# Kernel tuning notes

Measured on AMD Instinct MI355X. Metric: run time of the kernel, lower is better.

Reference implementation:

```python
import jax, jax.numpy as jnp
import numpy as np

B, S, EMB, HID, IMG, ATT, K, HL = 64, 512, 768, 512, 2048, 512, 6, 20


def setup_inputs() -> dict:
    key = jax.random.key(0)
    ks = jax.random.split(key, 14)
    u = lambda k, shape: jax.random.uniform(k, shape, jnp.float32, -0.1, 0.1)
    return {
        "representations": jax.random.normal(ks[0], (B, S, EMB), jnp.float32),
        "lengths": jax.random.randint(ks[1], (B,), 0, S),
        "separate_images": jax.random.normal(ks[2], (B, K, IMG), jnp.float32),
        "visual_context": jax.random.normal(ks[3], (B, K * IMG), jnp.float32),
        "prev_hist": jax.random.normal(ks[4], (B, K, HL, EMB), jnp.float32),
        "hist_counts": jax.random.randint(ks[5], (B, K), 0, HL + 1),
        "masks": jax.random.randint(ks[6], (B, S, 1), 0, 2).astype(bool),
        "W_sep": u(ks[7], (IMG, HID)), "b_sep": jnp.zeros((HID,), jnp.float32),
        "W_e2h": u(ks[8], (EMB, HID)), "b_e2h": jnp.zeros((HID,), jnp.float32),
        "W_hist": u(ks[9], (EMB, HID)), "b_hist": jnp.zeros((HID,), jnp.float32),
        "W_ctx": u(ks[10], (K * IMG, HID)), "b_ctx": jnp.zeros((HID,), jnp.float32),
        "W_mm": u(ks[11], (2 * HID, HID)), "b_mm": jnp.zeros((HID,), jnp.float32),
        "W_a1": u(ks[12], (HID, ATT)), "b_a1": jnp.zeros((ATT,), jnp.float32),
        "W_a2": u(ks[13], (ATT, 1)), "b_a2": jnp.zeros((1,), jnp.float32),
    }


def reference(representations, lengths, separate_images, visual_context,
              prev_hist, hist_counts, masks,
              W_sep, b_sep, W_e2h, b_e2h, W_hist, b_hist, W_ctx, b_ctx,
              W_mm, b_mm, W_a1, b_a1, W_a2, b_a2):
    # dropout_prob = 0 -> dropout is identity (eval-mode equivalence)
    input_reps = jax.nn.relu(representations @ W_e2h + b_e2h)          # [B,S,H]
    ctx = jax.nn.relu(visual_context @ W_ctx + b_ctx)                  # [B,H]
    ctx_rep = jnp.broadcast_to(ctx[:, None, :], input_reps.shape)
    mm = jax.nn.relu(jnp.concatenate([input_reps, ctx_rep], -1) @ W_mm + b_mm)  # [B,S,H]
    scores = jnp.tanh(mm @ W_a1 + b_a1) @ W_a2 + b_a2                  # [B,S,1]
    scores = jnp.where(masks, -jnp.inf, scores)
    att_w = jax.nn.softmax(scores, axis=1)                             # softmax over seq
    attended = jnp.sum(mm * att_w, axis=1)                             # [B,H]

    sep = separate_images @ W_sep + b_sep                              # [B,K,H]
    hl = prev_hist.shape[2]
    valid = jnp.arange(hl)[None, None, :] < hist_counts[:, :, None]    # [B,K,HL]
    hsum = jnp.sum(prev_hist * valid[..., None].astype(prev_hist.dtype), axis=2)
    havg = hsum / jnp.maximum(hist_counts, 1)[..., None].astype(prev_hist.dtype)
    hproj = jax.nn.relu(havg @ W_hist + b_hist)                        # [B,K,H]
    sep = sep + jnp.where((hist_counts > 0)[..., None], hproj, 0.0)
    sep = jax.nn.relu(sep)
    # F.normalize(p=2, dim=2, eps=1e-12)
    sep = sep / jnp.maximum(jnp.linalg.norm(sep, axis=2, keepdims=True), 1e-12)
    dot = jnp.einsum('bkh,bh->bk', sep, attended)[..., None]           # [B,K,1]
    return dot
```

## Files before the change

kernel.cpp:

```cpp
#include <hip/hip_runtime.h>
#include <math.h>

#define B_    64
#define S_    512
#define EMB_  768
#define HID_  512
#define IMG_  2048
#define ATT_  512
#define K_    6
#define HL_   20

typedef __attribute__((ext_vector_type(8))) short bf16x8;
typedef __attribute__((ext_vector_type(4))) float f32x4;

__device__ __forceinline__ unsigned short f2b(float f) {
    unsigned int u = __float_as_uint(f);
    u += 0x7fffu + ((u >> 16) & 1u);
    return (unsigned short)(u >> 16);
}
__device__ __forceinline__ float b2f(unsigned short s) {
    return __uint_as_float(((unsigned int)s) << 16);
}

#define GLD_LDS16(gp, lp)                                                        \
    __builtin_amdgcn_global_load_lds(                                            \
        (const __attribute__((address_space(1))) void*)(gp),                     \
        (__attribute__((address_space(3))) void*)(lp), 16, 0, 0)

__global__ __launch_bounds__(256)
void mask_detect(const unsigned char* __restrict__ m, int* __restrict__ flag, int nbytes) {
    __shared__ int found;
    if (threadIdx.x == 0) found = 0;
    __syncthreads();
    for (int i = threadIdx.x; i < nbytes; i += 256) {
        if ((i & 3) != 0 && m[i] != 0) found = 1;
    }
    __syncthreads();
    if (threadIdx.x == 0) *flag = found;
}

__global__ __launch_bounds__(256)
void cvt_f32_bf16(const float* __restrict__ in, unsigned short* __restrict__ out, int n8) {
    int stride = gridDim.x * 256;
    for (int i = blockIdx.x * 256 + threadIdx.x; i < n8; i += stride) {
        float4 a = ((const float4*)in)[i * 2];
        float4 b = ((const float4*)in)[i * 2 + 1];
        unsigned short r[8] = {f2b(a.x), f2b(a.y), f2b(a.z), f2b(a.w),
                               f2b(b.x), f2b(b.y), f2b(b.z), f2b(b.w)};
        ((uint4*)out)[i] = *(uint4*)r;
    }
}

__global__ __launch_bounds__(256)
void transpose_cvt(const float* __restrict__ W, unsigned short* __restrict__ Wt,
                   int Kd, int N) {
    __shared__ float tile[32][33];
    int k0 = blockIdx.x * 32, n0 = blockIdx.y * 32;
    int tx = threadIdx.x & 31, ty = threadIdx.x >> 5;
    #pragma unroll
    for (int i = 0; i < 4; ++i)
        tile[ty + i * 8][tx] = W[(size_t)(k0 + ty + i * 8) * N + n0 + tx];
    __syncthreads();
    #pragma unroll
    for (int i = 0; i < 4; ++i)
        Wt[(size_t)(n0 + ty + i * 8) * Kd + k0 + tx] = f2b(tile[tx][ty + i * 8]);
}

template<int ACT>
__global__ __launch_bounds__(256)
void gemm_bf16(const unsigned short* __restrict__ A, const unsigned short* __restrict__ Bt,
               const float* __restrict__ bias, const float* __restrict__ row_add,
               int row_div, unsigned short* __restrict__ Co, int M, int N, int Kd) {
    __shared__ unsigned short Als[2][128 * 64];
    __shared__ unsigned short Bls[2][128 * 64];
    const int tid = threadIdx.x;

    const int nwg = gridDim.x;
    const int cpx = nwg >> 3;
    const int lid = ((int)blockIdx.x & 7) * cpx + ((int)blockIdx.x >> 3);
    const int ntl = N >> 7;
    const int bn = (lid % ntl) << 7;
    const int bm = (lid / ntl) << 7;

    const int lane = tid & 63;
    const int wid = tid >> 6;
    const int wr = wid >> 1, wc = wid & 1;
    const int fr = lane & 15, hi = lane >> 4;

    f32x4 acc[4][4] = {};

    int srow[4], scol[4];
    #pragma unroll
    for (int c = 0; c < 4; ++c) {
        int g = c * 256 + tid;
        srow[c] = g >> 3;
        scol[c] = (g & 7) ^ (srow[c] & 7);
    }

    const int nt = Kd >> 6;
    #pragma unroll
    for (int c = 0; c < 4; ++c) {
        int g = c * 256 + tid;
        GLD_LDS16(A + (size_t)(bm + srow[c]) * Kd + scol[c] * 8, &Als[0][g * 8]);
        GLD_LDS16(Bt + (size_t)(bn + srow[c]) * Kd + scol[c] * 8, &Bls[0][g * 8]);
    }
    __syncthreads();

    for (int t = 0; t < nt; ++t) {
        const int buf = t & 1;
        if (t + 1 < nt) {
            const int k0 = (t + 1) << 6;
            #pragma unroll
            for (int c = 0; c < 4; ++c) {
                int g = c * 256 + tid;
                GLD_LDS16(A + (size_t)(bm + srow[c]) * Kd + k0 + scol[c] * 8,
                          &Als[buf ^ 1][g * 8]);
                GLD_LDS16(Bt + (size_t)(bn + srow[c]) * Kd + k0 + scol[c] * 8,
                          &Bls[buf ^ 1][g * 8]);
            }
        }
        #pragma unroll
        for (int kk = 0; kk < 2; ++kk) {
            bf16x8 af[4], bv[4];
            #pragma unroll
            for (int m = 0; m < 4; ++m) {
                int row = wr * 64 + m * 16 + fr;
                int sc = (kk * 4 + hi) ^ (fr & 7);
                af[m] = *(const bf16x8*)&Als[buf][row * 64 + sc * 8];
            }
            #pragma unroll
            for (int n = 0; n < 4; ++n) {
                int row = wc * 64 + n * 16 + fr;
                int sc = (kk * 4 + hi) ^ (fr & 7);
                bv[n] = *(const bf16x8*)&Bls[buf][row * 64 + sc * 8];
            }
            #pragma unroll
            for (int m = 0; m < 4; ++m)
                #pragma unroll
                for (int n = 0; n < 4; ++n)
                    acc[m][n] = __builtin_amdgcn_mfma_f32_16x16x32_bf16(af[m], bv[n], acc[m][n], 0, 0, 0);
        }
        __syncthreads();
    }

    const int rg = hi;
    #pragma unroll
    for (int m = 0; m < 4; ++m) {
        #pragma unroll
        for (int n = 0; n < 4; ++n) {
            int col = bn + wc * 64 + n * 16 + fr;
            float badd = bias ? bias[col] : 0.f;
            #pragma unroll
            for (int r = 0; r < 4; ++r) {
                int row = bm + wr * 64 + m * 16 + rg * 4 + r;
                float x = acc[m][n][r] + badd;
                if (row_add) x += row_add[(size_t)(row / row_div) * N + col];
                if (ACT == 1) x = fmaxf(x, 0.f);
                if (ACT == 2) x = tanhf(x);
                Co[(size_t)row * N + col] = f2b(x);
            }
        }
    }
}

__global__ __launch_bounds__(256)
void gemm_splitk(const float* __restrict__ A, const float* __restrict__ W,
                 float* __restrict__ P, int M, int N, int Kd, int kps) {
    __shared__ float As[16][68];
    __shared__ float Ws[16][64];
    const int tid = threadIdx.x;
    const int bm = blockIdx.y * 64, bn = blockIdx.x * 64;
    const int ks = blockIdx.z;
    const int tx = tid & 15, ty = tid >> 4;
    const int arow = tid >> 2, akq = tid & 3;
    const int wk = tid >> 4, wnq = tid & 15;

    float acc[4][4] = {};
    const int kbeg = ks * kps, kend = kbeg + kps;

    for (int k0 = kbeg; k0 < kend; k0 += 16) {
        float4 av = *(const float4*)&A[(size_t)(bm + arow) * Kd + k0 + akq * 4];
        float4 wv = *(const float4*)&W[(size_t)(k0 + wk) * N + bn + wnq * 4];
        As[akq * 4 + 0][arow] = av.x;
        As[akq * 4 + 1][arow] = av.y;
        As[akq * 4 + 2][arow] = av.z;
        As[akq * 4 + 3][arow] = av.w;
        *(float4*)&Ws[wk][wnq * 4] = wv;
        __syncthreads();
        #pragma unroll
        for (int kk = 0; kk < 16; ++kk) {
            float4 a4 = *(const float4*)&As[kk][ty * 4];
            float4 b4 = *(const float4*)&Ws[kk][tx * 4];
            float a_[4] = {a4.x, a4.y, a4.z, a4.w};
            float b_[4] = {b4.x, b4.y, b4.z, b4.w};
            #pragma unroll
            for (int i = 0; i < 4; ++i)
                #pragma unroll
                for (int j = 0; j < 4; ++j)
                    acc[i][j] += a_[i] * b_[j];
        }
        __syncthreads();
    }

    float* Pbase = P + (size_t)ks * M * N;
    #pragma unroll
    for (int i = 0; i < 4; ++i) {
        int row = bm + ty * 4 + i;
        float4 v = {acc[i][0], acc[i][1], acc[i][2], acc[i][3]};
        *(float4*)&Pbase[(size_t)row * N + bn + tx * 4] = v;
    }
}

template<int ACT>
__global__ __launch_bounds__(256)
void reduce_k(const float* __restrict__ P, const float* __restrict__ bias,
              float* __restrict__ C, int MN, int N, int nsplit) {
    int idx = blockIdx.x * 256 + threadIdx.x;
    if (idx >= MN) return;
    float s = 0.f;
    for (int z = 0; z < nsplit; ++z) s += P[(size_t)z * MN + idx];
    if (bias) s += bias[idx & (N - 1)];
    if (ACT == 1) s = fmaxf(s, 0.f);
    C[idx] = s;
}

__global__ __launch_bounds__(256)
void score_dot(const unsigned short* __restrict__ t, const float* __restrict__ W_a2,
               const float* __restrict__ b_a2, float* __restrict__ scores) {
    int row = blockIdx.x * 4 + (threadIdx.x >> 6);
    int lane = threadIdx.x & 63;
    const unsigned short* tr = t + (size_t)row * ATT_;
    float s = 0.f;
    #pragma unroll
    for (int i = 0; i < ATT_ / 64; ++i)
        s += b2f(tr[lane + i * 64]) * W_a2[lane + i * 64];
    #pragma unroll
    for (int off = 32; off; off >>= 1) s += __shfl_down(s, off, 64);
    if (lane == 0) scores[row] = s + b_a2[0];
}

__global__ __launch_bounds__(256)
void softmax_mask(float* __restrict__ scores, const void* __restrict__ masks_raw,
                  const int* __restrict__ flag) {
    int b = blockIdx.x, tid = threadIdx.x;
    bool isb = (*flag) != 0;
    const unsigned char* mb = (const unsigned char*)masks_raw;
    const int* mi = (const int*)masks_raw;
    int lane = tid & 63, wv = tid >> 6;
    __shared__ float red[4], red2[4];

    float m = -INFINITY;
    for (int s = tid; s < S_; s += 256) {
        int idx = b * S_ + s;
        bool mk = isb ? (mb[idx] != 0) : (mi[idx] != 0);
        float v = mk ? -INFINITY : scores[idx];
        scores[idx] = v;
        m = fmaxf(m, v);
    }
    #pragma unroll
    for (int off = 32; off; off >>= 1) m = fmaxf(m, __shfl_down(m, off, 64));
    if (lane == 0) red[wv] = m;
    __syncthreads();
    if (tid == 0) red[0] = fmaxf(fmaxf(red[0], red[1]), fmaxf(red[2], red[3]));
    __syncthreads();
    float Mx = red[0];

    float sum = 0.f;
    for (int s = tid; s < S_; s += 256) {
        int idx = b * S_ + s;
        float e = expf(scores[idx] - Mx);
        scores[idx] = e;
        sum += e;
    }
    #pragma unroll
    for (int off = 32; off; off >>= 1) sum += __shfl_down(sum, off, 64);
    if (lane == 0) red2[wv] = sum;
    __syncthreads();
    if (tid == 0) red2[0] = red2[0] + red2[1] + red2[2] + red2[3];
    __syncthreads();
    float inv = 1.f / red2[0];
    for (int s = tid; s < S_; s += 256) scores[b * S_ + s] *= inv;
}

__global__ __launch_bounds__(256)
void attended_k(const unsigned short* __restrict__ mm, const float* __restrict__ att_w,
                float* __restrict__ attended) {
    int b = blockIdx.x;
    int h = blockIdx.y * 256 + threadIdx.x;
    __shared__ float w[S_];
    for (int s = threadIdx.x; s < S_; s += 256) w[s] = att_w[b * S_ + s];
    __syncthreads();
    float acc = 0.f;
    for (int s = 0; s < S_; ++s)
        acc += b2f(mm[((size_t)b * S_ + s) * HID_ + h]) * w[s];
    attended[b * HID_ + h] = acc;
}

__global__ __launch_bounds__(256)
void hist_avg(const float* __restrict__ ph, const int* __restrict__ hcnt,
              float* __restrict__ havg) {
    int bk = blockIdx.x;
    int cnt = hcnt[bk];
    float denom = (float)(cnt > 1 ? cnt : 1);
    const float* base = ph + (size_t)bk * HL_ * EMB_;
    for (int e = threadIdx.x; e < EMB_; e += 256) {
        float s = 0.f;
        for (int l = 0; l < cnt; ++l) s += base[l * EMB_ + e];
        havg[bk * EMB_ + e] = s / denom;
    }
}

__global__ __launch_bounds__(256)
void combine(const float* __restrict__ sep0, const float* __restrict__ hproj,
             const int* __restrict__ hcnt, const float* __restrict__ attended,
             float* __restrict__ out) {
    int bk = blockIdx.x, tid = threadIdx.x;
    int b = bk / K_;
    int cnt = hcnt[bk];
    float sq = 0.f, dt = 0.f;
    #pragma unroll
    for (int i = 0; i < HID_ / 256; ++i) {
        int h = tid + i * 256;
        float v = sep0[bk * HID_ + h];
        if (cnt > 0) v += hproj[bk * HID_ + h];
        v = fmaxf(v, 0.f);
        sq += v * v;
        dt += v * attended[b * HID_ + h];
    }
    #pragma unroll
    for (int off = 32; off; off >>= 1) {
        sq += __shfl_down(sq, off, 64);
        dt += __shfl_down(dt, off, 64);
    }
    __shared__ float rs[4], rd[4];
    int lane = tid & 63, wv = tid >> 6;
    if (lane == 0) { rs[wv] = sq; rd[wv] = dt; }
    __syncthreads();
    if (tid == 0) {
        float Sq = rs[0] + rs[1] + rs[2] + rs[3];
        float Dt = rd[0] + rd[1] + rd[2] + rd[3];
        float norm = fmaxf(sqrtf(Sq), 1e-12f);
        out[bk] = Dt / norm;
    }
}

extern "C" void kernel_launch(void* const* d_in, const int* in_sizes, int n_in,
                              void* d_out, int out_size, void* d_ws, size_t ws_size,
                              hipStream_t stream) {
    const float* reps     = (const float*)d_in[0];
    const float* sep_imgs = (const float*)d_in[2];
    const float* vctx     = (const float*)d_in[3];
    const float* phist    = (const float*)d_in[4];
    const int*   hcnt     = (const int*)d_in[5];
    const void*  masks    = d_in[6];
    const float* W_sep = (const float*)d_in[7];
    const float* b_sep = (const float*)d_in[8];
    const float* W_e2h = (const float*)d_in[9];
    const float* b_e2h = (const float*)d_in[10];
    const float* W_hist = (const float*)d_in[11];
    const float* b_hist = (const float*)d_in[12];
    const float* W_ctx = (const float*)d_in[13];
    const float* b_ctx = (const float*)d_in[14];
    const float* W_mm = (const float*)d_in[15];
    const float* b_mm = (const float*)d_in[16];
    const float* W_a1 = (const float*)d_in[17];
    const float* b_a1 = (const float*)d_in[18];
    const float* W_a2 = (const float*)d_in[19];
    const float* b_a2 = (const float*)d_in[20];
    float* out = (float*)d_out;

    const size_t MS = (size_t)B_ * S_;

    unsigned short* repsb = (unsigned short*)d_ws;
    unsigned short* actA  = repsb + MS * EMB_;
    unsigned short* actB  = actA + MS * HID_;
    unsigned short* WtE2H = actB + MS * HID_;
    unsigned short* WtMM  = WtE2H + (size_t)EMB_ * HID_;
    unsigned short* WtA1  = WtMM + (size_t)HID_ * HID_;
    float* skbuf = (float*)(WtA1 + (size_t)HID_ * HID_);
    float* ctx   = skbuf + (size_t)16 * 384 * 512;
    float* ctx2  = ctx + B_ * HID_;
    float* scores = ctx2 + B_ * HID_;
    float* attended = scores + MS;
    float* sep0  = attended + B_ * HID_;
    float* havg  = sep0 + B_ * K_ * HID_;
    float* hproj = havg + B_ * K_ * EMB_;
    int*   flag  = (int*)(hproj + B_ * K_ * HID_);

    mask_detect<<<1, 256, 0, stream>>>((const unsigned char*)masks, flag, 8192);

    cvt_f32_bf16<<<2048, 256, 0, stream>>>(reps, repsb, (int)(MS * EMB_ / 8));
    transpose_cvt<<<dim3(EMB_ / 32, HID_ / 32), 256, 0, stream>>>(W_e2h, WtE2H, EMB_, HID_);
    transpose_cvt<<<dim3(HID_ / 32, HID_ / 32), 256, 0, stream>>>(W_mm, WtMM, HID_, HID_);
    transpose_cvt<<<dim3(HID_ / 32, HID_ / 32), 256, 0, stream>>>(W_a1, WtA1, HID_, HID_);

    {
        const int nsp = 64, kps = (K_ * IMG_) / nsp;
        gemm_splitk<<<dim3(8, 1, nsp), 256, 0, stream>>>(vctx, W_ctx, skbuf,
                                                         B_, HID_, K_ * IMG_, kps);
        reduce_k<1><<<(B_ * HID_ + 255) / 256, 256, 0, stream>>>(skbuf, b_ctx, ctx,
                                                                 B_ * HID_, HID_, nsp);
    }
    {
        const int nsp = 8, kps = HID_ / nsp;
        gemm_splitk<<<dim3(8, 1, nsp), 256, 0, stream>>>(ctx, W_mm + (size_t)HID_ * HID_,
                                                         skbuf, B_, HID_, HID_, kps);
        reduce_k<0><<<(B_ * HID_ + 255) / 256, 256, 0, stream>>>(skbuf, b_mm, ctx2,
                                                                 B_ * HID_, HID_, nsp);
    }
    const int big_grid = ((int)MS / 128) * (HID_ / 128);
    gemm_bf16<1><<<big_grid, 256, 0, stream>>>(repsb, WtE2H, b_e2h, nullptr, 1,
                                               actA, (int)MS, HID_, EMB_);
    gemm_bf16<1><<<big_grid, 256, 0, stream>>>(actA, WtMM, nullptr, ctx2, S_,
                                               actB, (int)MS, HID_, HID_);
    gemm_bf16<2><<<big_grid, 256, 0, stream>>>(actB, WtA1, b_a1, nullptr, 1,
                                               actA, (int)MS, ATT_, HID_);
    score_dot<<<8192, 256, 0, stream>>>(actA, W_a2, b_a2, scores);
    softmax_mask<<<B_, 256, 0, stream>>>(scores, masks, flag);
    attended_k<<<dim3(B_, HID_ / 256), 256, 0, stream>>>(actB, scores, attended);
    hist_avg<<<B_ * K_, 256, 0, stream>>>(phist, hcnt, havg);
    {
        const int nsp = 8, kps = EMB_ / nsp;
        gemm_splitk<<<dim3(8, 6, nsp), 256, 0, stream>>>(havg, W_hist, skbuf,
                                                         B_ * K_, HID_, EMB_, kps);
        reduce_k<1><<<(B_ * K_ * HID_ + 255) / 256, 256, 0, stream>>>(skbuf, b_hist, hproj,
                                                                      B_ * K_ * HID_, HID_, nsp);
    }
    {
        const int nsp = 16, kps = IMG_ / nsp;
        gemm_splitk<<<dim3(8, 6, nsp), 256, 0, stream>>>(sep_imgs, W_sep, skbuf,
                                                         B_ * K_, HID_, IMG_, kps);
        reduce_k<0><<<(B_ * K_ * HID_ + 255) / 256, 256, 0, stream>>>(skbuf, b_sep, sep0,
                                                                      B_ * K_ * HID_, HID_, nsp);
    }
    combine<<<B_ * K_, 256, 0, stream>>>(sep0, hproj, hcnt, attended, out);
}
```

Baseline: 316.2 us.

## Fuse bf16 conversion, score projection, split-k reductions and prep kernels

Removes the separate fp32-to-bf16 pass over the representations: the first GEMM now loads fp32 directly and converts to bf16 in registers before writing LDS. The tanh attention GEMM now folds the W_a2 dot into its epilogue and writes per-tile partial scores, so the [MS,512] tanh activation is never written and re-read. Softmax sums those partials, the attended reduction is split over four sequence chunks, and the hist/sep split-k reductions are merged into the final combine kernel. Weight transposes and mask detection are merged into one launch. This cuts launches and large memory traffic, but the fp32 A loads go through registers rather than direct-to-LDS and the epilogue does more tanh and shuffle work.

```diff
diff --git a/kernel.cpp b/kernel.cpp
--- a/kernel.cpp
+++ b/kernel.cpp
@@ -9,6 +9,7 @@
 #define ATT_  512
 #define K_    6
 #define HL_   20
+#define MS_   (B_ * S_)
 
 typedef __attribute__((ext_vector_type(8))) short bf16x8;
 typedef __attribute__((ext_vector_type(4))) float f32x4;
@@ -18,8 +19,10 @@
     u += 0x7fffu + ((u >> 16) & 1u);
     return (unsigned short)(u >> 16);
 }
-__device__ __forceinline__ float b2f(unsigned short s) {
-    return __uint_as_float(((unsigned int)s) << 16);
+__device__ __forceinline__ unsigned int pk_bf16(float lo, float hi) {
+    unsigned int r;
+    asm volatile("v_cvt_pk_bf16_f32 %0, %1, %2" : "=v"(r) : "v"(lo), "v"(hi));
+    return r;
 }
 
 #define GLD_LDS16(gp, lp)                                                        \
@@ -28,42 +31,50 @@
         (__attribute__((address_space(3))) void*)(lp), 16, 0, 0)
 
 __global__ __launch_bounds__(256)
-void mask_detect(const unsigned char* __restrict__ m, int* __restrict__ flag, int nbytes) {
-    __shared__ int found;
-    if (threadIdx.x == 0) found = 0;
-    __syncthreads();
-    for (int i = threadIdx.x; i < nbytes; i += 256) {
-        if ((i & 3) != 0 && m[i] != 0) found = 1;
-    }
-    __syncthreads();
-    if (threadIdx.x == 0) *flag = found;
-}
-
-__global__ __launch_bounds__(256)
-void cvt_f32_bf16(const float* __restrict__ in, unsigned short* __restrict__ out, int n8) {
-    int stride = gridDim.x * 256;
-    for (int i = blockIdx.x * 256 + threadIdx.x; i < n8; i += stride) {
-        float4 a = ((const float4*)in)[i * 2];
-        float4 b = ((const float4*)in)[i * 2 + 1];
-        unsigned short r[8] = {f2b(a.x), f2b(a.y), f2b(a.z), f2b(a.w),
-                               f2b(b.x), f2b(b.y), f2b(b.z), f2b(b.w)};
-        ((uint4*)out)[i] = *(uint4*)r;
-    }
-}
-
-__global__ __launch_bounds__(256)
-void transpose_cvt(const float* __restrict__ W, unsigned short* __restrict__ Wt,
-                   int Kd, int N) {
+void prep(const float* __restrict__ W_e2h, const float* __restrict__ W_mm,
+          const float* __restrict__ W_a1,
+          unsigned short* __restrict__ WtE2H, unsigned short* __restrict__ WtMM,
+          unsigned short* __restrict__ WtA1,
+          const unsigned char* __restrict__ masks, int* __restrict__ flag) {
+    const int z = blockIdx.z;
+    if (z == 3) {
+        if (blockIdx.x != 0 || blockIdx.y != 0) return;
+        __shared__ int found;
+        if (threadIdx.x == 0) found = 0;
+        __syncthreads();
+        for (int i = threadIdx.x; i < 8192; i += 256)
+            if ((i & 3) != 0 && masks[i] != 0) found = 1;
+        __syncthreads();
+        if (threadIdx.x == 0) *flag = found;
+        return;
+    }
+    const float* W;
+    unsigned short* Wt;
+    int Kd;
+    if (z == 0)      { W = W_e2h; Wt = WtE2H; Kd = EMB_; }
+    else if (z == 1) { W = W_mm;  Wt = WtMM;  Kd = HID_; }
+    else             { W = W_a1;  Wt = WtA1;  Kd = HID_; }
+    if ((int)blockIdx.x * 32 >= Kd) return;
+
     __shared__ float tile[32][33];
     int k0 = blockIdx.x * 32, n0 = blockIdx.y * 32;
     int tx = threadIdx.x & 31, ty = threadIdx.x >> 5;
     #pragma unroll
     for (int i = 0; i < 4; ++i)
-        tile[ty + i * 8][tx] = W[(size_t)(k0 + ty + i * 8) * N + n0 + tx];
+        tile[ty + i * 8][tx] = W[(size_t)(k0 + ty + i * 8) * HID_ + n0 + tx];
     __syncthreads();
     #pragma unroll
     for (int i = 0; i < 4; ++i)
         Wt[(size_t)(n0 + ty + i * 8) * Kd + k0 + tx] = f2b(tile[tx][ty + i * 8]);
+}
+
+__device__ __forceinline__ void tile_coords(int N, int& bm, int& bn) {
+    const int nwg = gridDim.x;
+    const int cpx = nwg >> 3;
+    const int lid = ((int)blockIdx.x & 7) * cpx + ((int)blockIdx.x >> 3);
+    const int ntl = N >> 7;
+    bn = (lid % ntl) << 7;
+    bm = (lid / ntl) << 7;
 }
 
 template<int ACT>
@@ -74,21 +85,12 @@
     __shared__ unsigned short Als[2][128 * 64];
     __shared__ unsigned short Bls[2][128 * 64];
     const int tid = threadIdx.x;
-
-    const int nwg = gridDim.x;
-    const int cpx = nwg >> 3;
-    const int lid = ((int)blockIdx.x & 7) * cpx + ((int)blockIdx.x >> 3);
-    const int ntl = N >> 7;
-    const int bn = (lid % ntl) << 7;
-    const int bm = (lid / ntl) << 7;
-
-    const int lane = tid & 63;
-    const int wid = tid >> 6;
+    int bm, bn; tile_coords(N, bm, bn);
+    const int lane = tid & 63, wid = tid >> 6;
     const int wr = wid >> 1, wc = wid & 1;
     const int fr = lane & 15, hi = lane >> 4;
 
     f32x4 acc[4][4] = {};
-
     int srow[4], scol[4];
     #pragma unroll
     for (int c = 0; c < 4; ++c) {
@@ -143,7 +145,6 @@
         __syncthreads();
     }
 
-    const int rg = hi;
     #pragma unroll
     for (int m = 0; m < 4; ++m) {
         #pragma unroll
@@ -152,13 +153,217 @@
             float badd = bias ? bias[col] : 0.f;
             #pragma unroll
             for (int r = 0; r < 4; ++r) {
-                int row = bm + wr * 64 + m * 16 + rg * 4 + r;
+                int row = bm + wr * 64 + m * 16 + hi * 4 + r;
                 float x = acc[m][n][r] + badd;
                 if (row_add) x += row_add[(size_t)(row / row_div) * N + col];
                 if (ACT == 1) x = fmaxf(x, 0.f);
                 if (ACT == 2) x = tanhf(x);
                 Co[(size_t)row * N + col] = f2b(x);
             }
+        }
+    }
+}
+
+template<int ACT>
+__global__ __launch_bounds__(256)
+void gemm_f32in(const float* __restrict__ A, const unsigned short* __restrict__ Bt,
+                const float* __restrict__ bias, unsigned short* __restrict__ Co,
+                int M, int N, int Kd) {
+    __shared__ unsigned short Als[2][128 * 64];
+    __shared__ unsigned short Bls[2][128 * 64];
+    const int tid = threadIdx.x;
+    int bm, bn; tile_coords(N, bm, bn);
+    const int lane = tid & 63, wid = tid >> 6;
+    const int wr = wid >> 1, wc = wid & 1;
+    const int fr = lane & 15, hi = lane >> 4;
+
+    f32x4 acc[4][4] = {};
+    int srow[4], lcol[4], scol[4];
+    #pragma unroll
+    for (int c = 0; c < 4; ++c) {
+        int g = c * 256 + tid;
+        srow[c] = g >> 3;
+        lcol[c] = g & 7;
+        scol[c] = lcol[c] ^ (srow[c] & 7);
+    }
+
+    const int nt = Kd >> 6;
+    float4 ra[8];
+
+    #pragma unroll
+    for (int c = 0; c < 4; ++c) {
+        int g = c * 256 + tid;
+        GLD_LDS16(Bt + (size_t)(bn + srow[c]) * Kd + scol[c] * 8, &Bls[0][g * 8]);
+        const float* p = A + (size_t)(bm + srow[c]) * Kd + lcol[c] * 8;
+        ra[2 * c]     = *(const float4*)p;
+        ra[2 * c + 1] = *(const float4*)(p + 4);
+    }
+    #pragma unroll
+    for (int c = 0; c < 4; ++c) {
+        uint4 u;
+        u.x = pk_bf16(ra[2*c].x,   ra[2*c].y);
+        u.y = pk_bf16(ra[2*c].z,   ra[2*c].w);
+        u.z = pk_bf16(ra[2*c+1].x, ra[2*c+1].y);
+        u.w = pk_bf16(ra[2*c+1].z, ra[2*c+1].w);
+        *(uint4*)&Als[0][(srow[c] * 8 + scol[c]) * 8] = u;
+    }
+    __syncthreads();
+
+    for (int t = 0; t < nt; ++t) {
+        const int buf = t & 1;
+        if (t + 1 < nt) {
+            const int k0 = (t + 1) << 6;
+            #pragma unroll
+            for (int c = 0; c < 4; ++c) {
+                int g = c * 256 + tid;
+                GLD_LDS16(Bt + (size_t)(bn + srow[c]) * Kd + k0 + scol[c] * 8,
+                          &Bls[buf ^ 1][g * 8]);
+                const float* p = A + (size_t)(bm + srow[c]) * Kd + k0 + lcol[c] * 8;
+                ra[2 * c]     = *(const float4*)p;
+                ra[2 * c + 1] = *(const float4*)(p + 4);
+            }
+        }
+        #pragma unroll
+        for (int kk = 0; kk < 2; ++kk) {
+            bf16x8 af[4], bv[4];
+            #pragma unroll
+            for (int m = 0; m < 4; ++m) {
+                int row = wr * 64 + m * 16 + fr;
+                int sc = (kk * 4 + hi) ^ (fr & 7);
+                af[m] = *(const bf16x8*)&Als[buf][row * 64 + sc * 8];
+            }
+            #pragma unroll
+            for (int n = 0; n < 4; ++n) {
+                int row = wc * 64 + n * 16 + fr;
+                int sc = (kk * 4 + hi) ^ (fr & 7);
+                bv[n] = *(const bf16x8*)&Bls[buf][row * 64 + sc * 8];
+            }
+            #pragma unroll
+            for (int m = 0; m < 4; ++m)
+                #pragma unroll
+                for (int n = 0; n < 4; ++n)
+                    acc[m][n] = __builtin_amdgcn_mfma_f32_16x16x32_bf16(af[m], bv[n], acc[m][n], 0, 0, 0);
+        }
+        if (t + 1 < nt) {
+            #pragma unroll
+            for (int c = 0; c < 4; ++c) {
+                uint4 u;
+                u.x = pk_bf16(ra[2*c].x,   ra[2*c].y);
+                u.y = pk_bf16(ra[2*c].z,   ra[2*c].w);
+                u.z = pk_bf16(ra[2*c+1].x, ra[2*c+1].y);
+                u.w = pk_bf16(ra[2*c+1].z, ra[2*c+1].w);
+                *(uint4*)&Als[buf ^ 1][(srow[c] * 8 + scol[c]) * 8] = u;
+            }
+        }
+        __syncthreads();
+    }
+
+    #pragma unroll
+    for (int m = 0; m < 4; ++m) {
+        #pragma unroll
+        for (int n = 0; n < 4; ++n) {
+            int col = bn + wc * 64 + n * 16 + fr;
+            float badd = bias ? bias[col] : 0.f;
+            #pragma unroll
+            for (int r = 0; r < 4; ++r) {
+                int row = bm + wr * 64 + m * 16 + hi * 4 + r;
+                float x = acc[m][n][r] + badd;
+                if (ACT == 1) x = fmaxf(x, 0.f);
+                Co[(size_t)row * N + col] = f2b(x);
+            }
+        }
+    }
+}
+
+__global__ __launch_bounds__(256)
+void gemm_score(const unsigned short* __restrict__ A, const unsigned short* __restrict__ Bt,
+                const float* __restrict__ b_a1, const float* __restrict__ W_a2,
+                float* __restrict__ scores8, int M, int N, int Kd) {
+    __shared__ unsigned short Als[2][128 * 64];
+    __shared__ unsigned short Bls[2][128 * 64];
+    const int tid = threadIdx.x;
+    int bm, bn; tile_coords(N, bm, bn);
+    const int lane = tid & 63, wid = tid >> 6;
+    const int wr = wid >> 1, wc = wid & 1;
+    const int fr = lane & 15, hi = lane >> 4;
+
+    f32x4 acc[4][4] = {};
+    int srow[4], scol[4];
+    #pragma unroll
+    for (int c = 0; c < 4; ++c) {
+        int g = c * 256 + tid;
+        srow[c] = g >> 3;
+        scol[c] = (g & 7) ^ (srow[c] & 7);
+    }
+
+    const int nt = Kd >> 6;
+    #pragma unroll
+    for (int c = 0; c < 4; ++c) {
+        int g = c * 256 + tid;
+        GLD_LDS16(A + (size_t)(bm + srow[c]) * Kd + scol[c] * 8, &Als[0][g * 8]);
+        GLD_LDS16(Bt + (size_t)(bn + srow[c]) * Kd + scol[c] * 8, &Bls[0][g * 8]);
+    }
+    __syncthreads();
+
+    for (int t = 0; t < nt; ++t) {
+        const int buf = t & 1;
+        if (t + 1 < nt) {
+            const int k0 = (t + 1) << 6;
+            #pragma unroll
+            for (int c = 0; c < 4; ++c) {
+                int g = c * 256 + tid;
+                GLD_LDS16(A + (size_t)(bm + srow[c]) * Kd + k0 + scol[c] * 8,
+                          &Als[buf ^ 1][g * 8]);
+                GLD_LDS16(Bt + (size_t)(bn + srow[c]) * Kd + k0 + scol[c] * 8,
+                          &Bls[buf ^ 1][g * 8]);
+            }
+        }
+        #pragma unroll
+        for (int kk = 0; kk < 2; ++kk) {
+            bf16x8 af[4], bv[4];
+            #pragma unroll
+            for (int m = 0; m < 4; ++m) {
+                int row = wr * 64 + m * 16 + fr;
+                int sc = (kk * 4 + hi) ^ (fr & 7);
+                af[m] = *(const bf16x8*)&Als[buf][row * 64 + sc * 8];
+            }
+            #pragma unroll
+            for (int n = 0; n < 4; ++n) {
+                int row = wc * 64 + n * 16 + fr;
+                int sc = (kk * 4 + hi) ^ (fr & 7);
+                bv[n] = *(const bf16x8*)&Bls[buf][row * 64 + sc * 8];
+            }
+            #pragma unroll
+            for (int m = 0; m < 4; ++m)
+                #pragma unroll
+                for (int n = 0; n < 4; ++n)
+                    acc[m][n] = __builtin_amdgcn_mfma_f32_16x16x32_bf16(af[m], bv[n], acc[m][n], 0, 0, 0);
+        }
+        __syncthreads();
+    }
+
+    float ba[4], wa[4];
+    #pragma unroll
+    for (int n = 0; n < 4; ++n) {
+        int col = bn + wc * 64 + n * 16 + fr;
+        ba[n] = b_a1[col];
+        wa[n] = W_a2[col];
+    }
+    const int slot = (bn >> 7) * 2 + wc;
+    #pragma unroll
+    for (int m = 0; m < 4; ++m) {
+        #pragma unroll
+        for (int r = 0; r < 4; ++r) {
+            float p = 0.f;
+            #pragma unroll
+            for (int n = 0; n < 4; ++n)
+                p += tanhf(acc[m][n][r] + ba[n]) * wa[n];
+            p += __shfl_xor(p, 1, 64);
+            p += __shfl_xor(p, 2, 64);
+            p += __shfl_xor(p, 4, 64);
+            p += __shfl_xor(p, 8, 64);
+            if (fr == 0)
+                scores8[(size_t)slot * M + bm + wr * 64 + m * 16 + hi * 4 + r] = p;
         }
     }
 }
@@ -225,36 +430,26 @@
 }
 
 __global__ __launch_bounds__(256)
-void score_dot(const unsigned short* __restrict__ t, const float* __restrict__ W_a2,
-               const float* __restrict__ b_a2, float* __restrict__ scores) {
-    int row = blockIdx.x * 4 + (threadIdx.x >> 6);
-    int lane = threadIdx.x & 63;
-    const unsigned short* tr = t + (size_t)row * ATT_;
-    float s = 0.f;
-    #pragma unroll
-    for (int i = 0; i < ATT_ / 64; ++i)
-        s += b2f(tr[lane + i * 64]) * W_a2[lane + i * 64];
-    #pragma unroll
-    for (int off = 32; off; off >>= 1) s += __shfl_down(s, off, 64);
-    if (lane == 0) scores[row] = s + b_a2[0];
-}
-
-__global__ __launch_bounds__(256)
-void softmax_mask(float* __restrict__ scores, const void* __restrict__ masks_raw,
-                  const int* __restrict__ flag) {
+void softmax8(const float* __restrict__ scores8, const float* __restrict__ b_a2,
+              const void* __restrict__ masks_raw, const int* __restrict__ flag,
+              float* __restrict__ attw) {
     int b = blockIdx.x, tid = threadIdx.x;
     bool isb = (*flag) != 0;
     const unsigned char* mb = (const unsigned char*)masks_raw;
     const int* mi = (const int*)masks_raw;
     int lane = tid & 63, wv = tid >> 6;
     __shared__ float red[4], red2[4];
+    float bias = b_a2[0];
 
     float m = -INFINITY;
     for (int s = tid; s < S_; s += 256) {
         int idx = b * S_ + s;
+        float v = bias;
+        #pragma unroll
+        for (int z = 0; z < 8; ++z) v += scores8[(size_t)z * MS_ + idx];
         bool mk = isb ? (mb[idx] != 0) : (mi[idx] != 0);
-        float v = mk ? -INFINITY : scores[idx];
-        scores[idx] = v;
+        v = mk ? -INFINITY : v;
+        attw[idx] = v;
         m = fmaxf(m, v);
     }
     #pragma unroll
@@ -268,8 +463,8 @@
     float sum = 0.f;
     for (int s = tid; s < S_; s += 256) {
         int idx = b * S_ + s;
-        float e = expf(scores[idx] - Mx);
-        scores[idx] = e;
+        float e = expf(attw[idx] - Mx);
+        attw[idx] = e;
         sum += e;
     }
     #pragma unroll
@@ -279,21 +474,23 @@
     if (tid == 0) red2[0] = red2[0] + red2[1] + red2[2] + red2[3];
     __syncthreads();
     float inv = 1.f / red2[0];
-    for (int s = tid; s < S_; s += 256) scores[b * S_ + s] *= inv;
-}
-
-__global__ __launch_bounds__(256)
-void attended_k(const unsigned short* __restrict__ mm, const float* __restrict__ att_w,
-                float* __restrict__ attended) {
+    for (int s = tid; s < S_; s += 256) attw[b * S_ + s] *= inv;
+}
+
+__global__ __launch_bounds__(256)
+void attended4(const unsigned short* __restrict__ mm, const float* __restrict__ attw,
+               float* __restrict__ att4) {
     int b = blockIdx.x;
     int h = blockIdx.y * 256 + threadIdx.x;
-    __shared__ float w[S_];
-    for (int s = threadIdx.x; s < S_; s += 256) w[s] = att_w[b * S_ + s];
+    int z = blockIdx.z;
+    __shared__ float w[128];
+    int s0 = z * 128;
+    if (threadIdx.x < 128) w[threadIdx.x] = attw[b * S_ + s0 + threadIdx.x];
     __syncthreads();
     float acc = 0.f;
-    for (int s = 0; s < S_; ++s)
-        acc += b2f(mm[((size_t)b * S_ + s) * HID_ + h]) * w[s];
-    attended[b * HID_ + h] = acc;
+    for (int s = 0; s < 128; ++s)
+        acc += __uint_as_float((unsigned int)mm[((size_t)b * S_ + s0 + s) * HID_ + h] << 16) * w[s];
+    att4[((size_t)z * B_ + b) * HID_ + h] = acc;
 }
 
 __global__ __launch_bounds__(256)
@@ -311,9 +508,11 @@
 }
 
 __global__ __launch_bounds__(256)
-void combine(const float* __restrict__ sep0, const float* __restrict__ hproj,
-             const int* __restrict__ hcnt, const float* __restrict__ attended,
-             float* __restrict__ out) {
+void combine_all(const float* __restrict__ skA, const float* __restrict__ skB,
+                 const float* __restrict__ b_hist, const float* __restrict__ b_sep,
+                 const int* __restrict__ hcnt, const float* __restrict__ att4,
+                 float* __restrict__ out) {
+    const int MNA = B_ * K_ * HID_;
     int bk = blockIdx.x, tid = threadIdx.x;
     int b = bk / K_;
     int cnt = hcnt[bk];
@@ -321,11 +520,21 @@
     #pragma unroll
     for (int i = 0; i < HID_ / 256; ++i) {
         int h = tid + i * 256;
-        float v = sep0[bk * HID_ + h];
-        if (cnt > 0) v += hproj[bk * HID_ + h];
+        size_t idx = (size_t)bk * HID_ + h;
+        float hp = b_hist[h];
+        #pragma unroll
+        for (int z = 0; z < 8; ++z) hp += skA[(size_t)z * MNA + idx];
+        hp = fmaxf(hp, 0.f);
+        float sp = b_sep[h];
+        #pragma unroll
+        for (int z = 0; z < 16; ++z) sp += skB[(size_t)z * MNA + idx];
+        float v = sp + (cnt > 0 ? hp : 0.f);
         v = fmaxf(v, 0.f);
+        float at = 0.f;
+        #pragma unroll
+        for (int z = 0; z < 4; ++z) at += att4[((size_t)z * B_ + b) * HID_ + h];
         sq += v * v;
-        dt += v * attended[b * HID_ + h];
+        dt += v * at;
     }
     #pragma unroll
     for (int off = 32; off; off >>= 1) {
@@ -369,69 +578,57 @@
     const float* b_a2 = (const float*)d_in[20];
     float* out = (float*)d_out;
 
-    const size_t MS = (size_t)B_ * S_;
-
-    unsigned short* repsb = (unsigned short*)d_ws;
-    unsigned short* actA  = repsb + MS * EMB_;
+    const size_t MS = (size_t)MS_;
+    const int MNA = B_ * K_ * HID_;
+
+    unsigned short* actA  = (unsigned short*)d_ws;
     unsigned short* actB  = actA + MS * HID_;
     unsigned short* WtE2H = actB + MS * HID_;
     unsigned short* WtMM  = WtE2H + (size_t)EMB_ * HID_;
     unsigned short* WtA1  = WtMM + (size_t)HID_ * HID_;
-    float* skbuf = (float*)(WtA1 + (size_t)HID_ * HID_);
-    float* ctx   = skbuf + (size_t)16 * 384 * 512;
-    float* ctx2  = ctx + B_ * HID_;
-    float* scores = ctx2 + B_ * HID_;
-    float* attended = scores + MS;
-    float* sep0  = attended + B_ * HID_;
-    float* havg  = sep0 + B_ * K_ * HID_;
-    float* hproj = havg + B_ * K_ * EMB_;
-    int*   flag  = (int*)(hproj + B_ * K_ * HID_);
-
-    mask_detect<<<1, 256, 0, stream>>>((const unsigned char*)masks, flag, 8192);
-
-    cvt_f32_bf16<<<2048, 256, 0, stream>>>(reps, repsb, (int)(MS * EMB_ / 8));
-    transpose_cvt<<<dim3(EMB_ / 32, HID_ / 32), 256, 0, stream>>>(W_e2h, WtE2H, EMB_, HID_);
-    transpose_cvt<<<dim3(HID_ / 32, HID_ / 32), 256, 0, stream>>>(W_mm, WtMM, HID_, HID_);
-    transpose_cvt<<<dim3(HID_ / 32, HID_ / 32), 256, 0, stream>>>(W_a1, WtA1, HID_, HID_);
+    float* skC    = (float*)(WtA1 + (size_t)HID_ * HID_);
+    float* skA    = skC + (size_t)64 * B_ * HID_;
+    float* skB    = skA + (size_t)8 * MNA;
+    float* scores8 = skB + (size_t)16 * MNA;
+    float* attw   = scores8 + 8 * MS;
+    float* att4   = attw + MS;
+    float* ctx    = att4 + (size_t)4 * B_ * HID_;
+    float* ctx2   = ctx + B_ * HID_;
+    float* havg   = ctx2 + B_ * HID_;
+    int*   flag   = (int*)(havg + (size_t)B_ * K_ * EMB_);
+
+    prep<<<dim3(EMB_ / 32, HID_ / 32, 4), 256, 0, stream>>>(
+        W_e2h, W_mm, W_a1, WtE2H, WtMM, WtA1, (const unsigned char*)masks, flag);
 
     {
         const int nsp = 64, kps = (K_ * IMG_) / nsp;
-        gemm_splitk<<<dim3(8, 1, nsp), 256, 0, stream>>>(vctx, W_ctx, skbuf,
+        gemm_splitk<<<dim3(8, 1, nsp), 256, 0, stream>>>(vctx, W_ctx, skC,
                                                          B_, HID_, K_ * IMG_, kps);
-        reduce_k<1><<<(B_ * HID_ + 255) / 256, 256, 0, stream>>>(skbuf, b_ctx, ctx,
+        reduce_k<1><<<(B_ * HID_ + 255) / 256, 256, 0, stream>>>(skC, b_ctx, ctx,
                                                                  B_ * HID_, HID_, nsp);
     }
     {
         const int nsp = 8, kps = HID_ / nsp;
         gemm_splitk<<<dim3(8, 1, nsp), 256, 0, stream>>>(ctx, W_mm + (size_t)HID_ * HID_,
-                                                         skbuf, B_, HID_, HID_, kps);
-        reduce_k<0><<<(B_ * HID_ + 255) / 256, 256, 0, stream>>>(skbuf, b_mm, ctx2,
+                                                         skC, B_, HID_, HID_, kps);
+        reduce_k<0><<<(B_ * HID_ + 255) / 256, 256, 0, stream>>>(skC, b_mm, ctx2,
                                                                  B_ * HID_, HID_, nsp);
     }
-    const int big_grid = ((int)MS / 128) * (HID_ / 128);
-    gemm_bf16<1><<<big_grid, 256, 0, stream>>>(repsb, WtE2H, b_e2h, nullptr, 1,
-                                               actA, (int)MS, HID_, EMB_);
+
+    const int big_grid = (MS_ / 128) * (HID_ / 128);
+    gemm_f32in<1><<<big_grid, 256, 0, stream>>>(reps, WtE2H, b_e2h, actA,
+                                                MS_, HID_, EMB_);
     gemm_bf16<1><<<big_grid, 256, 0, stream>>>(actA, WtMM, nullptr, ctx2, S_,
-                                               actB, (int)MS, HID_, HID_);
-    gemm_bf16<2><<<big_grid, 256, 0, stream>>>(actB, WtA1, b_a1, nullptr, 1,
-                                               actA, (int)MS, ATT_, HID_);
-    score_dot<<<8192, 256, 0, stream>>>(actA, W_a2, b_a2, scores);
-    softmax_mask<<<B_, 256, 0, stream>>>(scores, masks, flag);
-    attended_k<<<dim3(B_, HID_ / 256), 256, 0, stream>>>(actB, scores, attended);
+                                               actB, MS_, HID_, HID_);
+    gemm_score<<<big_grid, 256, 0, stream>>>(actB, WtA1, b_a1, W_a2, scores8,
+                                             MS_, ATT_, HID_);
+    softmax8<<<B_, 256, 0, stream>>>(scores8, b_a2, masks, flag, attw);
+    attended4<<<dim3(B_, HID_ / 256, 4), 256, 0, stream>>>(actB, attw, att4);
     hist_avg<<<B_ * K_, 256, 0, stream>>>(phist, hcnt, havg);
-    {
-        const int nsp = 8, kps = EMB_ / nsp;
-        gemm_splitk<<<dim3(8, 6, nsp), 256, 0, stream>>>(havg, W_hist, skbuf,
-                                                         B_ * K_, HID_, EMB_, kps);
-        reduce_k<1><<<(B_ * K_ * HID_ + 255) / 256, 256, 0, stream>>>(skbuf, b_hist, hproj,
-                                                                      B_ * K_ * HID_, HID_, nsp);
-    }
-    {
-        const int nsp = 16, kps = IMG_ / nsp;
-        gemm_splitk<<<dim3(8, 6, nsp), 256, 0, stream>>>(sep_imgs, W_sep, skbuf,
-                                                         B_ * K_, HID_, IMG_, kps);
-        reduce_k<0><<<(B_ * K_ * HID_ + 255) / 256, 256, 0, stream>>>(skbuf, b_sep, sep0,
-                                                                      B_ * K_ * HID_, HID_, nsp);
-    }
-    combine<<<B_ * K_, 256, 0, stream>>>(sep0, hproj, hcnt, attended, out);
-}
+    gemm_splitk<<<dim3(8, 6, 8), 256, 0, stream>>>(havg, W_hist, skA,
+                                                   B_ * K_, HID_, EMB_, EMB_ / 8);
+    gemm_splitk<<<dim3(8, 6, 16), 256, 0, stream>>>(sep_imgs, W_sep, skB,
+                                                    B_ * K_, HID_, IMG_, IMG_ / 16);
+    combine_all<<<B_ * K_, 256, 0, stream>>>(skA, skB, b_hist, b_sep, hcnt,
+                                             att4, out);
+}
```

Measured after the change: 262.7 us. 1.2x faster.
